# Optimization experiments

Measured on AMD Instinct MI355X. Metric: run time of the kernel, lower is better.

Reference implementation:

```python
import jax, jax.numpy as jnp
import numpy as np

# Deformable Conv v2 (modulated) config matching init_kwargs
KH, KW = 3, 3
STRIDE = (1, 1)
PAD = (1, 1)
DIL = (1, 1)


def _deform_conv2d(input, offset, mask, weight, bias):
    """Modulated deformable conv2d (DCNv2), deformable_groups=1.

    input:  [B, C, H, W]
    offset: [B, 2*K, Ho, Wo]  (y, x) interleaved per kernel tap
    mask:   [B, K, Ho, Wo]
    weight: [O, C, KH, KW]
    bias:   [O]
    """
    B, C, H, W = input.shape
    O = weight.shape[0]
    K = KH * KW
    sh, sw = STRIDE
    ph, pw = PAD
    dh, dw = DIL
    Ho = (H + 2 * ph - dh * (KH - 1) - 1) // sh + 1
    Wo = (W + 2 * pw - dw * (KW - 1) - 1) // sw + 1
    dt = input.dtype

    # Base sampling grid per kernel tap: [K, Ho, Wo] (broadcasted)
    ky, kx = jnp.meshgrid(jnp.arange(KH), jnp.arange(KW), indexing='ij')
    ky = ky.reshape(K).astype(dt)
    kx = kx.reshape(K).astype(dt)
    base_y = (jnp.arange(Ho, dtype=dt) * sh - ph)[None, :, None] + (ky * dh)[:, None, None]
    base_x = (jnp.arange(Wo, dtype=dt) * sw - pw)[None, None, :] + (kx * dw)[:, None, None]

    off = offset.reshape(B, K, 2, Ho, Wo)
    y = base_y[None] + off[:, :, 0]  # [B, K, Ho, Wo]
    x = base_x[None] + off[:, :, 1]

    y0 = jnp.floor(y)
    x0 = jnp.floor(x)
    wy = y - y0  # fractional parts
    wx = x - x0

    flat = input.reshape(B, C, H * W)

    def gather(yi, xi):
        # zero padding outside the image
        valid = ((yi >= 0) & (yi < H) & (xi >= 0) & (xi < W)).astype(dt)
        yc = jnp.clip(yi, 0, H - 1).astype(jnp.int32)
        xc = jnp.clip(xi, 0, W - 1).astype(jnp.int32)
        idx = (yc * W + xc).reshape(B, 1, K * Ho * Wo)
        v = jnp.take_along_axis(flat, jnp.broadcast_to(idx, (B, C, K * Ho * Wo)), axis=2)
        return v.reshape(B, C, K, Ho, Wo) * valid[:, None]

    g00 = gather(y0, x0)
    g01 = gather(y0, x0 + 1)
    g10 = gather(y0 + 1, x0)
    g11 = gather(y0 + 1, x0 + 1)

    wy = wy[:, None]  # [B, 1, K, Ho, Wo]
    wx = wx[:, None]
    val = (g00 * (1 - wy) * (1 - wx) + g01 * (1 - wy) * wx
           + g10 * wy * (1 - wx) + g11 * wy * wx)
    val = val * mask[:, None]  # modulation

    out = jnp.einsum('bckq,ock->boq', val.reshape(B, C, K, Ho * Wo),
                     weight.reshape(O, C, K))
    return out.reshape(B, O, Ho, Wo) + bias[None, :, None, None]


def setup_inputs() -> dict:
    key = jax.random.key(0)
    k1, k2, k3, k4, k5 = jax.random.split(key, 5)
    B, C, H, W = 8, 64, 96, 96
    O = 64
    K = KH * KW
    input = jax.random.normal(k1, (B, C, H, W), dtype=jnp.float32)
    offset = jax.random.normal(k2, (B, 2 * K, H, W), dtype=jnp.float32)
    mask = jax.random.uniform(k3, (B, K, H, W), dtype=jnp.float32)
    fan_in = C * KH * KW
    bound = 1.0 / np.sqrt(fan_in)
    weight = jax.random.uniform(k4, (O, C, KH, KW), minval=-bound, maxval=bound, dtype=jnp.float32)
    bias = jax.random.uniform(k5, (O,), minval=-bound, maxval=bound, dtype=jnp.float32)
    return {"input": input, "offset": offset, "mask": mask, "weight": weight, "bias": bias}


def reference(input, offset, mask, weight, bias):
    return _deform_conv2d(input, offset, mask, weight, bias)
```

## Files before the change

### kernel.cpp

```cpp
#include <hip/hip_runtime.h>
#include <stdint.h>

#define Hs 96
#define Ws 96
#define HW 9216

typedef _Float16 h2 __attribute__((ext_vector_type(2)));
typedef _Float16 f16x8 __attribute__((ext_vector_type(8)));
typedef float f32x4 __attribute__((ext_vector_type(4)));

__device__ __forceinline__ unsigned interp4(h2 w00, h2 w01, h2 w10, h2 w11,
                                            unsigned a, unsigned bq, unsigned c,
                                            unsigned d) {
  h2 r = w10 * __builtin_bit_cast(h2, c) + w11 * __builtin_bit_cast(h2, d);
  r = w01 * __builtin_bit_cast(h2, bq) + r;
  r = w00 * __builtin_bit_cast(h2, a) + r;
  return __builtin_bit_cast(unsigned, r);
}

__global__ __launch_bounds__(256) void k_prep(const float* __restrict__ in,
                                              _Float16* __restrict__ cl,
                                              const float* __restrict__ w,
                                              _Float16* __restrict__ wg) {
  __shared__ _Float16 lt[32 * 68];
  int tid = threadIdx.x;
  int blk = blockIdx.x;
  if (blk >= 2304) {
    int i = (blk - 2304) * 256 + tid;
    int o = i / 576;
    int r = i - o * 576;
    int t = r >> 6, c = r & 63;
    wg[((size_t)(t * 8 + (c >> 3)) * 64 + o) * 8 + (c & 7)] =
        (_Float16)w[(o * 64 + c) * 9 + t];
    return;
  }
  int xt = blk % 3;
  int rr = blk / 3;
  int y = rr % Hs;
  int b = rr / Hs;
  int x0 = xt * 32;
  {
    int xx = tid & 31, cc = tid >> 5;
    const float* src = in + (size_t)b * 64 * HW + y * Ws + x0 + xx;
#pragma unroll
    for (int i = 0; i < 8; ++i) {
      int c = cc * 8 + i;
      lt[xx * 68 + c] = (_Float16)src[(size_t)c * HW];
    }
  }
  __syncthreads();
  {
    int c4 = tid & 15, pg = tid >> 4;
    _Float16* dst = cl + ((size_t)(b * Hs + y) * Ws + x0) * 64 + c4 * 4;
#pragma unroll
    for (int i = 0; i < 2; ++i) {
      int x = pg * 2 + i;
      *(uint2*)(dst + (size_t)x * 64) = *(const uint2*)(lt + x * 68 + c4 * 4);
    }
  }
}

__global__ __launch_bounds__(256, 5) void k_fused(
    const _Float16* __restrict__ incl, const float* __restrict__ off,
    const float* __restrict__ msk, const _Float16* __restrict__ wg,
    const float* __restrict__ bias, float* __restrict__ out) {
  __shared__ unsigned preA[576];
  __shared__ uint4 preW[576];
  __shared__ uint4 Vb[2][64 * 9];

  int tid = threadIdx.x;
  int blk = blockIdx.x;
  int b = blk & 7;
  int q0 = (blk >> 3) * 64;

  for (int i = tid; i < 576; i += 256) {
    int t = i >> 6, p = i & 63;
    int q = q0 + p;
    int qy = (int)(((unsigned)q * 43691u) >> 22);
    int qx = q - qy * 96;
    int ty = t / 3, tx = t - ty * 3;
    float dy = off[(size_t)(b * 18 + 2 * t) * HW + q];
    float dx = off[(size_t)(b * 18 + 2 * t + 1) * HW + q];
    float mv = msk[(size_t)(b * 9 + t) * HW + q];
    float yf = (float)(qy - 1 + ty) + dy;
    float xf = (float)(qx - 1 + tx) + dx;
    float y0f = floorf(yf), x0f = floorf(xf);
    float wy = yf - y0f, wx = xf - x0f;
    int y0 = (int)y0f, x0i = (int)x0f;
    int y1 = y0 + 1, x1 = x0i + 1;
    bool yv0 = (y0 >= 0) && (y0 < Hs);
    bool yv1 = (y1 >= 0) && (y1 < Hs);
    bool xv0 = (x0i >= 0) && (x0i < Ws);
    bool xv1 = (x1 >= 0) && (x1 < Ws);
    int y0c = min(max(y0, 0), Hs - 1), y1c = min(max(y1, 0), Hs - 1);
    int x0c = min(max(x0i, 0), Ws - 1), x1c = min(max(x1, 0), Ws - 1);
    float omy = 1.f - wy, omx = 1.f - wx;
    float f00 = omy * omx * mv * ((yv0 && xv0) ? 1.f : 0.f);
    float f01 = omy * wx  * mv * ((yv0 && xv1) ? 1.f : 0.f);
    float f10 = wy  * omx * mv * ((yv1 && xv0) ? 1.f : 0.f);
    float f11 = wy  * wx  * mv * ((yv1 && xv1) ? 1.f : 0.f);
    preA[i] = ((unsigned)(b * HW + y0c * 96 + x0c) * 128u) |
              (unsigned)(x1c - x0c) | ((unsigned)(y1c - y0c) << 1);
    uint4 pw;
    pw.x = __builtin_bit_cast(unsigned, __builtin_amdgcn_cvt_pkrtz(f00, f00));
    pw.y = __builtin_bit_cast(unsigned, __builtin_amdgcn_cvt_pkrtz(f01, f01));
    pw.z = __builtin_bit_cast(unsigned, __builtin_amdgcn_cvt_pkrtz(f10, f10));
    pw.w = __builtin_bit_cast(unsigned, __builtin_amdgcn_cvt_pkrtz(f11, f11));
    preW[i] = pw;
  }
  __syncthreads();

  int j = tid & 7;
  int g = tid >> 3;
  int lane = tid & 63, wv = tid >> 6;
  int n16 = lane & 15, q4 = lane >> 4;
  const char* inb = (const char*)incl;
  const uint4* Ag = (const uint4*)wg;
  int arow = wv * 16 + n16;

  f32x4 acc[4];
#pragma unroll
  for (int pg = 0; pg < 4; ++pg) {
    f32x4 z = {0.f, 0.f, 0.f, 0.f};
    acc[pg] = z;
  }

  uint4 ga[2][4];
  uint4 afn0, afn1;

#define ISSUE_GATHERS(T)                                                     \
  _Pragma("unroll") for (int it = 0; it < 2; ++it) {                         \
    int gg = g + it * 32;                                                    \
    unsigned ax = preA[(T) * 64 + gg];                                       \
    int a00 = (int)(ax & ~127u) + j * 16;                                    \
    int a01 = a00 + ((ax & 1) << 7);                                         \
    int a10 = a00 + ((ax & 2) * 6144);                                       \
    int a11 = a10 + ((ax & 1) << 7);                                         \
    ga[it][0] = *(const uint4*)(inb + a00);                                  \
    ga[it][1] = *(const uint4*)(inb + a01);                                  \
    ga[it][2] = *(const uint4*)(inb + a10);                                  \
    ga[it][3] = *(const uint4*)(inb + a11);                                  \
  }

  ISSUE_GATHERS(0)
  afn0 = Ag[(size_t)((0 + q4) * 64 + arow)];
  afn1 = Ag[(size_t)((4 + q4) * 64 + arow)];

#pragma unroll
  for (int t = 0; t < 9; ++t) {
    int buf = t & 1;
    uint4 v0, v1;
#pragma unroll
    for (int it = 0; it < 2; ++it) {
      int gg = g + it * 32;
      uint4 pw = preW[t * 64 + gg];
      h2 w00 = __builtin_bit_cast(h2, pw.x);
      h2 w01 = __builtin_bit_cast(h2, pw.y);
      h2 w10 = __builtin_bit_cast(h2, pw.z);
      h2 w11 = __builtin_bit_cast(h2, pw.w);
      uint4 r;
      r.x = interp4(w00, w01, w10, w11, ga[it][0].x, ga[it][1].x, ga[it][2].x, ga[it][3].x);
      r.y = interp4(w00, w01, w10, w11, ga[it][0].y, ga[it][1].y, ga[it][2].y, ga[it][3].y);
      r.z = interp4(w00, w01, w10, w11, ga[it][0].z, ga[it][1].z, ga[it][2].z, ga[it][3].z);
      r.w = interp4(w00, w01, w10, w11, ga[it][0].w, ga[it][1].w, ga[it][2].w, ga[it][3].w);
      if (it == 0) v0 = r; else v1 = r;
    }
    uint4 afc0 = afn0, afc1 = afn1;
    Vb[buf][g * 9 + j] = v0;
    Vb[buf][(g + 32) * 9 + j] = v1;
    __syncthreads();
    if (t < 8) {
      ISSUE_GATHERS(t + 1)
      afn0 = Ag[(size_t)(((t + 1) * 8 + q4) * 64 + arow)];
      afn1 = Ag[(size_t)(((t + 1) * 8 + 4 + q4) * 64 + arow)];
    }
#pragma unroll
    for (int pg = 0; pg < 4; ++pg) {
      f16x8 b0 = __builtin_bit_cast(f16x8, Vb[buf][(pg * 16 + n16) * 9 + q4]);
      f16x8 b1 = __builtin_bit_cast(f16x8, Vb[buf][(pg * 16 + n16) * 9 + 4 + q4]);
      acc[pg] = __builtin_amdgcn_mfma_f32_16x16x32_f16(
          __builtin_bit_cast(f16x8, afc0), b0, acc[pg], 0, 0, 0);
      acc[pg] = __builtin_amdgcn_mfma_f32_16x16x32_f16(
          __builtin_bit_cast(f16x8, afc1), b1, acc[pg], 0, 0, 0);
    }
  }
#undef ISSUE_GATHERS

  int m0 = wv * 16 + q4 * 4;
  float bv[4];
#pragma unroll
  for (int r = 0; r < 4; ++r) bv[r] = bias[m0 + r];
#pragma unroll
  for (int pg = 0; pg < 4; ++pg) {
    int col = q0 + pg * 16 + n16;
    float* op = out + (size_t)b * 64 * HW + col;
#pragma unroll
    for (int r = 0; r < 4; ++r)
      op[(size_t)(m0 + r) * HW] = acc[pg][r] + bv[r];
  }
}

extern "C" void kernel_launch(void* const* d_in, const int* in_sizes, int n_in,
                              void* d_out, int out_size, void* d_ws, size_t ws_size,
                              hipStream_t stream) {
  const float* input = (const float*)d_in[0];
  const float* offset = (const float*)d_in[1];
  const float* mask = (const float*)d_in[2];
  const float* weight = (const float*)d_in[3];
  const float* bias = (const float*)d_in[4];
  float* out = (float*)d_out;

  _Float16* incl = (_Float16*)d_ws;
  _Float16* wg = (_Float16*)((char*)d_ws + 9437184);

  k_prep<<<dim3(2448), dim3(256), 0, stream>>>(input, incl, weight, wg);
  k_fused<<<dim3(1152), dim3(256), 0, stream>>>(incl, offset, mask, wg, bias, out);
}
```

Measured before the change: 100.4 us.

## Interpolate directly into MFMA B-fragments, removing LDS staging and per-tap barriers

The fused kernel drops from 256 to 128 threads per block. Each lane now gathers and interpolates exactly the 8 channels it needs as an MFMA B operand, so the bilinear samples no longer go through a shared-memory buffer with a __syncthreads per tap. The K loop is split into 18 half-tap stages with register double-buffering of the gathers and weight fragments, and each wave computes all 64 output channels for 32 pixels. In exchange, more weight fragments are loaded per wave, register pressure rises (launch bounds 128,3), and there are fewer threads to hide gather latency.

```diff
diff --git a/kernel.cpp b/kernel.cpp
--- a/kernel.cpp
+++ b/kernel.cpp
@@ -60,20 +60,19 @@
   }
 }
 
-__global__ __launch_bounds__(256, 5) void k_fused(
+__global__ __launch_bounds__(128, 3) void k_fused(
     const _Float16* __restrict__ incl, const float* __restrict__ off,
     const float* __restrict__ msk, const _Float16* __restrict__ wg,
     const float* __restrict__ bias, float* __restrict__ out) {
   __shared__ unsigned preA[576];
   __shared__ uint4 preW[576];
-  __shared__ uint4 Vb[2][64 * 9];
 
   int tid = threadIdx.x;
   int blk = blockIdx.x;
   int b = blk & 7;
   int q0 = (blk >> 3) * 64;
 
-  for (int i = tid; i < 576; i += 256) {
+  for (int i = tid; i < 576; i += 128) {
     int t = i >> 6, p = i & 63;
     int q = q0 + p;
     int qy = (int)(((unsigned)q * 43691u) >> 22);
@@ -110,93 +109,91 @@
   }
   __syncthreads();
 
-  int j = tid & 7;
-  int g = tid >> 3;
-  int lane = tid & 63, wv = tid >> 6;
+  int lane = tid & 63, w = tid >> 6;
   int n16 = lane & 15, q4 = lane >> 4;
   const char* inb = (const char*)incl;
   const uint4* Ag = (const uint4*)wg;
-  int arow = wv * 16 + n16;
-
-  f32x4 acc[4];
-#pragma unroll
-  for (int pg = 0; pg < 4; ++pg) {
-    f32x4 z = {0.f, 0.f, 0.f, 0.f};
-    acc[pg] = z;
-  }
-
-  uint4 ga[2][4];
-  uint4 afn0, afn1;
-
-#define ISSUE_GATHERS(T)                                                     \
-  _Pragma("unroll") for (int it = 0; it < 2; ++it) {                         \
-    int gg = g + it * 32;                                                    \
-    unsigned ax = preA[(T) * 64 + gg];                                       \
-    int a00 = (int)(ax & ~127u) + j * 16;                                    \
-    int a01 = a00 + ((ax & 1) << 7);                                         \
-    int a10 = a00 + ((ax & 2) * 6144);                                       \
-    int a11 = a10 + ((ax & 1) << 7);                                         \
-    ga[it][0] = *(const uint4*)(inb + a00);                                  \
-    ga[it][1] = *(const uint4*)(inb + a01);                                  \
-    ga[it][2] = *(const uint4*)(inb + a10);                                  \
-    ga[it][3] = *(const uint4*)(inb + a11);                                  \
-  }
-
-  ISSUE_GATHERS(0)
-  afn0 = Ag[(size_t)((0 + q4) * 64 + arow)];
-  afn1 = Ag[(size_t)((4 + q4) * 64 + arow)];
-
-#pragma unroll
-  for (int t = 0; t < 9; ++t) {
-    int buf = t & 1;
-    uint4 v0, v1;
-#pragma unroll
-    for (int it = 0; it < 2; ++it) {
-      int gg = g + it * 32;
-      uint4 pw = preW[t * 64 + gg];
+  int pp0 = (w * 2) * 16 + n16;
+  int pp1 = (w * 2 + 1) * 16 + n16;
+
+  f32x4 acc[2][4];
+#pragma unroll
+  for (int pgi = 0; pgi < 2; ++pgi)
+#pragma unroll
+    for (int mt = 0; mt < 4; ++mt) {
+      f32x4 z = {0.f, 0.f, 0.f, 0.f};
+      acc[pgi][mt] = z;
+    }
+
+  uint4 af[2][4];
+  uint4 ga[2][2][4];
+
+#define LOADK(T, KC, BB)                                                      \
+  {                                                                           \
+    _Pragma("unroll") for (int mt = 0; mt < 4; ++mt)                          \
+        af[BB][mt] =                                                          \
+            Ag[(size_t)(((T) * 8 + (KC) * 4 + q4) * 64 + mt * 16 + n16)];     \
+    _Pragma("unroll") for (int pgi = 0; pgi < 2; ++pgi) {                     \
+      int p_ = pgi ? pp1 : pp0;                                               \
+      unsigned ax = preA[(T) * 64 + p_];                                      \
+      int a00 = (int)(ax & ~127u) + (KC) * 64 + q4 * 16;                      \
+      int a01 = a00 + ((ax & 1) << 7);                                        \
+      int a10 = a00 + ((ax & 2) * 6144);                                      \
+      int a11 = a10 + ((ax & 1) << 7);                                        \
+      ga[BB][pgi][0] = *(const uint4*)(inb + a00);                            \
+      ga[BB][pgi][1] = *(const uint4*)(inb + a01);                            \
+      ga[BB][pgi][2] = *(const uint4*)(inb + a10);                            \
+      ga[BB][pgi][3] = *(const uint4*)(inb + a11);                            \
+    }                                                                         \
+  }
+
+  LOADK(0, 0, 0)
+
+#pragma unroll
+  for (int s = 0; s < 18; ++s) {
+    const int buf = s & 1;
+    if (s < 17) {
+      const int sn = s + 1;
+      LOADK(sn >> 1, sn & 1, buf ^ 1)
+    }
+    const int t = s >> 1;
+#pragma unroll
+    for (int pgi = 0; pgi < 2; ++pgi) {
+      uint4 pw = preW[t * 64 + (pgi ? pp1 : pp0)];
       h2 w00 = __builtin_bit_cast(h2, pw.x);
       h2 w01 = __builtin_bit_cast(h2, pw.y);
       h2 w10 = __builtin_bit_cast(h2, pw.z);
       h2 w11 = __builtin_bit_cast(h2, pw.w);
-      uint4 r;
-      r.x = interp4(w00, w01, w10, w11, ga[it][0].x, ga[it][1].x, ga[it][2].x, ga[it][3].x);
-      r.y = interp4(w00, w01, w10, w11, ga[it][0].y, ga[it][1].y, ga[it][2].y, ga[it][3].y);
-      r.z = interp4(w00, w01, w10, w11, ga[it][0].z, ga[it][1].z, ga[it][2].z, ga[it][3].z);
-      r.w = interp4(w00, w01, w10, w11, ga[it][0].w, ga[it][1].w, ga[it][2].w, ga[it][3].w);
-      if (it == 0) v0 = r; else v1 = r;
-    }
-    uint4 afc0 = afn0, afc1 = afn1;
-    Vb[buf][g * 9 + j] = v0;
-    Vb[buf][(g + 32) * 9 + j] = v1;
-    __syncthreads();
-    if (t < 8) {
-      ISSUE_GATHERS(t + 1)
-      afn0 = Ag[(size_t)(((t + 1) * 8 + q4) * 64 + arow)];
-      afn1 = Ag[(size_t)(((t + 1) * 8 + 4 + q4) * 64 + arow)];
-    }
-#pragma unroll
-    for (int pg = 0; pg < 4; ++pg) {
-      f16x8 b0 = __builtin_bit_cast(f16x8, Vb[buf][(pg * 16 + n16) * 9 + q4]);
-      f16x8 b1 = __builtin_bit_cast(f16x8, Vb[buf][(pg * 16 + n16) * 9 + 4 + q4]);
-      acc[pg] = __builtin_amdgcn_mfma_f32_16x16x32_f16(
-          __builtin_bit_cast(f16x8, afc0), b0, acc[pg], 0, 0, 0);
-      acc[pg] = __builtin_amdgcn_mfma_f32_16x16x32_f16(
-          __builtin_bit_cast(f16x8, afc1), b1, acc[pg], 0, 0, 0);
-    }
-  }
-#undef ISSUE_GATHERS
-
-  int m0 = wv * 16 + q4 * 4;
-  float bv[4];
-#pragma unroll
-  for (int r = 0; r < 4; ++r) bv[r] = bias[m0 + r];
-#pragma unroll
-  for (int pg = 0; pg < 4; ++pg) {
-    int col = q0 + pg * 16 + n16;
+      uint4 bfu;
+      bfu.x = interp4(w00, w01, w10, w11, ga[buf][pgi][0].x, ga[buf][pgi][1].x,
+                      ga[buf][pgi][2].x, ga[buf][pgi][3].x);
+      bfu.y = interp4(w00, w01, w10, w11, ga[buf][pgi][0].y, ga[buf][pgi][1].y,
+                      ga[buf][pgi][2].y, ga[buf][pgi][3].y);
+      bfu.z = interp4(w00, w01, w10, w11, ga[buf][pgi][0].z, ga[buf][pgi][1].z,
+                      ga[buf][pgi][2].z, ga[buf][pgi][3].z);
+      bfu.w = interp4(w00, w01, w10, w11, ga[buf][pgi][0].w, ga[buf][pgi][1].w,
+                      ga[buf][pgi][2].w, ga[buf][pgi][3].w);
+      f16x8 bf = __builtin_bit_cast(f16x8, bfu);
+#pragma unroll
+      for (int mt = 0; mt < 4; ++mt)
+        acc[pgi][mt] = __builtin_amdgcn_mfma_f32_16x16x32_f16(
+            __builtin_bit_cast(f16x8, af[buf][mt]), bf, acc[pgi][mt], 0, 0, 0);
+    }
+  }
+#undef LOADK
+
+#pragma unroll
+  for (int pgi = 0; pgi < 2; ++pgi) {
+    int col = q0 + (w * 2 + pgi) * 16 + n16;
     float* op = out + (size_t)b * 64 * HW + col;
 #pragma unroll
-    for (int r = 0; r < 4; ++r)
-      op[(size_t)(m0 + r) * HW] = acc[pg][r] + bv[r];
+    for (int mt = 0; mt < 4; ++mt) {
+#pragma unroll
+      for (int r = 0; r < 4; ++r) {
+        int m = mt * 16 + q4 * 4 + r;
+        op[(size_t)m * HW] = acc[pgi][mt][r] + bias[m];
+      }
+    }
   }
 }
 
@@ -214,5 +211,5 @@
   _Float16* wg = (_Float16*)((char*)d_ws + 9437184);
 
   k_prep<<<dim3(2448), dim3(256), 0, stream>>>(input, incl, weight, wg);
-  k_fused<<<dim3(1152), dim3(256), 0, stream>>>(incl, offset, mask, wg, bias, out);
-}
+  k_fused<<<dim3(1152), dim3(128), 0, stream>>>(incl, offset, mask, wg, bias, out);
+}
```

Result: slower. 129.5 us (+29.0%).
